# Kernel optimization log

Measured on AMD Instinct MI355X. Metric: run time of the kernel, lower is better.

The kernel has to match this reference:

```python
import jax, jax.numpy as jnp
import numpy as np

B, H, I, E, K = 512, 1024, 1024, 32, 4
EPS, ALPHA, LIMIT = 1e-5, 1.702, 7.0


def _swiglu(h):
    # interleaved split: even cols -> glu path, odd cols -> linear path
    x_glu = jnp.minimum(h[..., ::2], LIMIT)
    x_lin = jnp.clip(h[..., 1::2], -LIMIT, LIMIT)
    return x_glu * jax.nn.sigmoid(ALPHA * x_glu) * (x_lin + 1.0)


def setup_inputs() -> dict:
    key = jax.random.key(0)
    ks = jax.random.split(key, 7)
    n = lambda k, shape, s: jax.random.normal(k, shape, dtype=jnp.float32) * s
    return {
        "x": n(ks[0], (B, H), 1.0),
        "norm_scale": jnp.ones((H,), jnp.float32),
        "gate_w": n(ks[1], (E, H), 0.02),
        "gate_b": n(ks[2], (E,), 0.02),
        "mlp1_w": n(ks[3], (E, 2 * I, H), 0.02),
        "mlp1_b": n(ks[4], (E, 2 * I), 0.02),
        "mlp2_w": n(ks[5], (E, H, I), 0.02),
        "mlp2_b": n(ks[6], (E, H), 0.02),
    }


def reference(x, norm_scale, gate_w, gate_b, mlp1_w, mlp1_b, mlp2_w, mlp2_b):
    # RMSNorm in fp32
    t = x * jax.lax.rsqrt(jnp.mean(x * x, axis=-1, keepdims=True) + EPS) * norm_scale
    # gate + top-k routing; softmax over the k selected logits
    g = t @ gate_w.T + gate_b                      # [B, E]
    vals, idx = jax.lax.top_k(g, K)                # [B, K]
    w = jax.nn.softmax(vals, axis=-1)              # [B, K]
    # dense routing weights [B, E]: w_dense[b, e] = sum_k w[b,k] * (idx[b,k]==e)
    w_dense = jnp.zeros((t.shape[0], gate_w.shape[0]), t.dtype)
    w_dense = w_dense.at[jnp.arange(t.shape[0])[:, None], idx].add(w)
    # grouped-dense equivalent of the per-token gathered einsum:
    # original: einsum('beck,bk->bec', mlp1_w[idx], t); here we compute all
    # experts densely and combine with w_dense (zero for unselected experts),
    # which is the same math without materializing [B,K,2I,H] weights.
    h = jnp.einsum('bk,eck->bec', t, mlp1_w) + mlp1_b   # [B, E, 2I]
    a = _swiglu(h)                                       # [B, E, I]
    o = jnp.einsum('bei,ehi->beh', a, mlp2_w) + mlp2_b   # [B, E, H]
    y = jnp.einsum('beh,be->bh', o, w_dense)             # [B, H]
    return x + y
```

## Files before the change

kernel.cpp:

```cpp
#include <hip/hip_runtime.h>
#include <hip/hip_bf16.h>
#include <math.h>


#define NB   512
#define NH   1024
#define NI   1024
#define NE   32
#define NK   4
#define N2I  2048
#define CAP  512

static constexpr float EPS   = 1e-5f;
static constexpr float ALPHA = 1.702f;
static constexpr float LIMIT = 7.0f;

typedef short bf16x8 __attribute__((ext_vector_type(8)));
typedef float f32x4  __attribute__((ext_vector_type(4)));

__device__ __forceinline__ short hi16(float x) {
    return (short)(__float_as_uint(x) >> 16);
}
__device__ __forceinline__ short lo16(float x) {
    unsigned hb = __float_as_uint(x) & 0xFFFF0000u;
    float r = x - __uint_as_float(hb);
    return (short)(__float_as_uint(r) >> 16);
}
__device__ __forceinline__ void cvt8r(float4 v0, float4 v1,
                                      bf16x8& hh, bf16x8& ll) {
    float f[8] = {v0.x, v0.y, v0.z, v0.w, v1.x, v1.y, v1.z, v1.w};
#pragma unroll
    for (int i = 0; i < 8; i++) { hh[i] = hi16(f[i]); ll[i] = lo16(f[i]); }
}

__global__ __launch_bounds__(256) void k_rms_gate(
    const float* __restrict__ x, const float* __restrict__ scale,
    const float* __restrict__ gw, const float* __restrict__ gb,
    float* __restrict__ t, int* __restrict__ cnt,
    int* __restrict__ tok, int* __restrict__ tke, float* __restrict__ tkw) {
    __shared__ float sh_t[NH];
    __shared__ float sh_red[4];
    __shared__ float sh_g[NE];
    const int b = blockIdx.x, tid = threadIdx.x;
    const int lane = tid & 63, wid = tid >> 6;

    float4 xv = reinterpret_cast<const float4*>(x + (size_t)b * NH)[tid];
    float ss = xv.x * xv.x + xv.y * xv.y + xv.z * xv.z + xv.w * xv.w;
#pragma unroll
    for (int o = 32; o >= 1; o >>= 1) ss += __shfl_down(ss, o);
    if (lane == 0) sh_red[wid] = ss;
    __syncthreads();
    const float tot = sh_red[0] + sh_red[1] + sh_red[2] + sh_red[3];
    const float r = rsqrtf(tot * (1.0f / NH) + EPS);
    float4 sv = reinterpret_cast<const float4*>(scale)[tid];
    float4 tv;
    tv.x = xv.x * r * sv.x; tv.y = xv.y * r * sv.y;
    tv.z = xv.z * r * sv.z; tv.w = xv.w * r * sv.w;
    reinterpret_cast<float4*>(sh_t)[tid] = tv;
    reinterpret_cast<float4*>(t + (size_t)b * NH)[tid] = tv;
    __syncthreads();

#pragma unroll
    for (int q = 0; q < 8; q++) {
        const int e = wid * 8 + q;
        const float* __restrict__ w = gw + (size_t)e * NH;
        float p = 0.f;
#pragma unroll
        for (int i = 0; i < 16; i++) { int k = lane + 64 * i; p += sh_t[k] * w[k]; }
#pragma unroll
        for (int o = 32; o >= 1; o >>= 1) p += __shfl_down(p, o);
        if (lane == 0) sh_g[e] = p + gb[e];
    }
    __syncthreads();

    if (tid == 0) {
        float gv[NE];
#pragma unroll
        for (int e = 0; e < NE; e++) gv[e] = sh_g[e];
        float vals[NK]; int ids[NK];
#pragma unroll
        for (int k = 0; k < NK; k++) {
            int bi = 0; float bv = gv[0];
            for (int e = 1; e < NE; e++) if (gv[e] > bv) { bv = gv[e]; bi = e; }
            vals[k] = bv; ids[k] = bi; gv[bi] = -1e30f;
        }
        const float m = vals[0];
        float s = 0.f, wv[NK];
#pragma unroll
        for (int k = 0; k < NK; k++) { wv[k] = __expf(vals[k] - m); s += wv[k]; }
        const float inv = 1.f / s;
#pragma unroll
        for (int k = 0; k < NK; k++) {
            const int e = ids[k];
            const int pos = atomicAdd(&cnt[e], 1);
            tok[e * CAP + pos] = b;
            tke[b * NK + k] = (e << 16) | pos;
            tkw[b * NK + k] = wv[k] * inv;
        }
    }
}

__global__ void k_prefix(const int* __restrict__ cnt, int* __restrict__ base) {
    if (threadIdx.x == 0) {
        int r = 0;
        for (int e = 0; e < NE; e++) { base[e] = r; r += cnt[e]; }
    }
}

__global__ __launch_bounds__(256, 2) void k_mlp1(
    const float* __restrict__ t, const float* __restrict__ w1,
    const float* __restrict__ b1, const int* __restrict__ cnt,
    const int* __restrict__ base, const int* __restrict__ tok,
    float* __restrict__ a) {
    const int e  = blockIdx.z;
    const int ne = cnt[e];
    const int m0 = blockIdx.y * 128;
    if (m0 >= ne) return;
    const int c0 = blockIdx.x * 128;
    const float* __restrict__ W = w1 + (size_t)e * N2I * NH + (size_t)c0 * NH;

    __shared__ short Ah[128][72], Al[128][72];
    __shared__ short Bh[128][72], Bl[128][72];
    __shared__ int   toks[128];

    const int tid = threadIdx.x;
    if (tid < 128) toks[tid] = (m0 + tid < ne) ? tok[e * CAP + m0 + tid] : -1;
    __syncthreads();

    const int lane = tid & 63;
    const int wv   = tid >> 6;
    const int wr = wv >> 1, wc = wv & 1;
    const int frow = lane & 15;
    const int fk   = (lane >> 4) * 8;
    const int sr = tid >> 3;
    const int sg = (tid & 7) * 8;

    f32x4 acc[4][4] = {};
    float4 ra[4][2], rb[4][2];
    int tkr[4];

#pragma unroll
    for (int p = 0; p < 4; p++) {
        const int r = sr + 32 * p;
        const int tk = toks[r]; tkr[p] = tk;
        const float* src = t + (size_t)(tk < 0 ? 0 : tk) * NH + sg;
        ra[p][0] = *(const float4*)src;
        ra[p][1] = *(const float4*)(src + 4);
        const float* wsrc = W + (size_t)r * NH + sg;
        rb[p][0] = *(const float4*)wsrc;
        rb[p][1] = *(const float4*)(wsrc + 4);
    }

    for (int k0 = 0; k0 < NH; k0 += 64) {
#pragma unroll
        for (int p = 0; p < 4; p++) {
            const int r = sr + 32 * p;
            bf16x8 hh, ll;
            cvt8r(ra[p][0], ra[p][1], hh, ll);
            if (tkr[p] < 0) {
#pragma unroll
                for (int i = 0; i < 8; i++) { hh[i] = 0; ll[i] = 0; }
            }
            *(bf16x8*)&Ah[r][sg] = hh;
            *(bf16x8*)&Al[r][sg] = ll;
            cvt8r(rb[p][0], rb[p][1], hh, ll);
            *(bf16x8*)&Bh[r][sg] = hh;
            *(bf16x8*)&Bl[r][sg] = ll;
        }
        if (k0 + 64 < NH) {
            const int kn = k0 + 64;
#pragma unroll
            for (int p = 0; p < 4; p++) {
                const int r = sr + 32 * p;
                const int tk = tkr[p];
                const float* src = t + (size_t)(tk < 0 ? 0 : tk) * NH + kn + sg;
                ra[p][0] = *(const float4*)src;
                ra[p][1] = *(const float4*)(src + 4);
                const float* wsrc = W + (size_t)r * NH + kn + sg;
                rb[p][0] = *(const float4*)wsrc;
                rb[p][1] = *(const float4*)(wsrc + 4);
            }
        }
        __syncthreads();
#pragma unroll
        for (int kk = 0; kk < 64; kk += 32) {
            bf16x8 ah[4], al[4], bh[4], bl[4];
#pragma unroll
            for (int m = 0; m < 4; m++) {
                const int r = wr * 64 + m * 16 + frow;
                ah[m] = *(const bf16x8*)&Ah[r][kk + fk];
                al[m] = *(const bf16x8*)&Al[r][kk + fk];
            }
#pragma unroll
            for (int n = 0; n < 4; n++) {
                const int c = wc * 64 + n * 16 + frow;
                bh[n] = *(const bf16x8*)&Bh[c][kk + fk];
                bl[n] = *(const bf16x8*)&Bl[c][kk + fk];
            }
#pragma unroll
            for (int m = 0; m < 4; m++)
#pragma unroll
                for (int n = 0; n < 4; n++) {
                    acc[m][n] = __builtin_amdgcn_mfma_f32_16x16x32_bf16(ah[m], bh[n], acc[m][n], 0, 0, 0);
                    acc[m][n] = __builtin_amdgcn_mfma_f32_16x16x32_bf16(ah[m], bl[n], acc[m][n], 0, 0, 0);
                    acc[m][n] = __builtin_amdgcn_mfma_f32_16x16x32_bf16(al[m], bh[n], acc[m][n], 0, 0, 0);
                }
        }
        __syncthreads();
    }

    const int slot0 = base[e];
#pragma unroll
    for (int m = 0; m < 4; m++)
#pragma unroll
        for (int n = 0; n < 4; n++) {
            const int gcol = c0 + wc * 64 + n * 16 + frow;
            const float bias = b1[e * N2I + gcol];
            f32x4 v = acc[m][n];
#pragma unroll
            for (int j = 0; j < 4; j++) {
                const float h  = v[j] + bias;
                const float hp = __shfl_xor(h, 1);
                const int row = m0 + wr * 64 + m * 16 + (lane >> 4) * 4 + j;
                if (!(lane & 1) && row < ne) {
                    const float xg = fminf(h, LIMIT);
                    const float xl = fminf(fmaxf(hp, -LIMIT), LIMIT);
                    const float sg2 = 1.f / (1.f + __expf(-ALPHA * xg));
                    a[(size_t)(slot0 + row) * NI + (gcol >> 1)] = xg * sg2 * (xl + 1.f);
                }
            }
        }
}

__global__ __launch_bounds__(256, 2) void k_mlp2(
    const float* __restrict__ a, const float* __restrict__ w2,
    const float* __restrict__ b2, const int* __restrict__ cnt,
    const int* __restrict__ base, float* __restrict__ o) {
    const int e  = blockIdx.z;
    const int ne = cnt[e];
    const int m0 = blockIdx.y * 128;
    if (m0 >= ne) return;
    const int c0 = blockIdx.x * 128;
    const int slot0 = base[e];
    const float* __restrict__ W = w2 + (size_t)e * NH * NI + (size_t)c0 * NI;

    __shared__ short Ah[128][72], Al[128][72];
    __shared__ short Bh[128][72], Bl[128][72];

    const int tid = threadIdx.x;
    const int lane = tid & 63;
    const int wv   = tid >> 6;
    const int wr = wv >> 1, wc = wv & 1;
    const int frow = lane & 15;
    const int fk   = (lane >> 4) * 8;
    const int sr = tid >> 3;
    const int sg = (tid & 7) * 8;

    f32x4 acc[4][4] = {};
    float4 ra[4][2], rb[4][2];
    int mv[4];

#pragma unroll
    for (int p = 0; p < 4; p++) {
        const int r = sr + 32 * p;
        const int m = m0 + r;
        mv[p] = (m < ne);
        const float* src = a + (size_t)(mv[p] ? (slot0 + m) : 0) * NI + sg;
        ra[p][0] = *(const float4*)src;
        ra[p][1] = *(const float4*)(src + 4);
        const float* wsrc = W + (size_t)r * NI + sg;
        rb[p][0] = *(const float4*)wsrc;
        rb[p][1] = *(const float4*)(wsrc + 4);
    }

    for (int k0 = 0; k0 < NI; k0 += 64) {
#pragma unroll
        for (int p = 0; p < 4; p++) {
            const int r = sr + 32 * p;
            bf16x8 hh, ll;
            cvt8r(ra[p][0], ra[p][1], hh, ll);
            if (!mv[p]) {
#pragma unroll
                for (int i = 0; i < 8; i++) { hh[i] = 0; ll[i] = 0; }
            }
            *(bf16x8*)&Ah[r][sg] = hh;
            *(bf16x8*)&Al[r][sg] = ll;
            cvt8r(rb[p][0], rb[p][1], hh, ll);
            *(bf16x8*)&Bh[r][sg] = hh;
            *(bf16x8*)&Bl[r][sg] = ll;
        }
        if (k0 + 64 < NI) {
            const int kn = k0 + 64;
#pragma unroll
            for (int p = 0; p < 4; p++) {
                const int r = sr + 32 * p;
                const int m = m0 + r;
                const float* src = a + (size_t)(mv[p] ? (slot0 + m) : 0) * NI + kn + sg;
                ra[p][0] = *(const float4*)src;
                ra[p][1] = *(const float4*)(src + 4);
                const float* wsrc = W + (size_t)r * NI + kn + sg;
                rb[p][0] = *(const float4*)wsrc;
                rb[p][1] = *(const float4*)(wsrc + 4);
            }
        }
        __syncthreads();
#pragma unroll
        for (int kk = 0; kk < 64; kk += 32) {
            bf16x8 ah[4], al[4], bh[4], bl[4];
#pragma unroll
            for (int m = 0; m < 4; m++) {
                const int r = wr * 64 + m * 16 + frow;
                ah[m] = *(const bf16x8*)&Ah[r][kk + fk];
                al[m] = *(const bf16x8*)&Al[r][kk + fk];
            }
#pragma unroll
            for (int n = 0; n < 4; n++) {
                const int c = wc * 64 + n * 16 + frow;
                bh[n] = *(const bf16x8*)&Bh[c][kk + fk];
                bl[n] = *(const bf16x8*)&Bl[c][kk + fk];
            }
#pragma unroll
            for (int m = 0; m < 4; m++)
#pragma unroll
                for (int n = 0; n < 4; n++) {
                    acc[m][n] = __builtin_amdgcn_mfma_f32_16x16x32_bf16(ah[m], bh[n], acc[m][n], 0, 0, 0);
                    acc[m][n] = __builtin_amdgcn_mfma_f32_16x16x32_bf16(ah[m], bl[n], acc[m][n], 0, 0, 0);
                    acc[m][n] = __builtin_amdgcn_mfma_f32_16x16x32_bf16(al[m], bh[n], acc[m][n], 0, 0, 0);
                }
        }
        __syncthreads();
    }

#pragma unroll
    for (int m = 0; m < 4; m++)
#pragma unroll
        for (int n = 0; n < 4; n++) {
            const int gcol = c0 + wc * 64 + n * 16 + frow;
            const float bias = b2[e * NH + gcol];
            f32x4 v = acc[m][n];
#pragma unroll
            for (int j = 0; j < 4; j++) {
                const int row = m0 + wr * 64 + m * 16 + (lane >> 4) * 4 + j;
                if (row < ne)
                    o[(size_t)(slot0 + row) * NH + gcol] = v[j] + bias;
            }
        }
}

__global__ __launch_bounds__(256) void k_combine(
    const float* __restrict__ x, const float* __restrict__ o,
    const int* __restrict__ base, const int* __restrict__ tke,
    const float* __restrict__ tkw, float* __restrict__ out) {
    const int b = blockIdx.x, tid = threadIdx.x;
    int slots[NK]; float wk[NK];
#pragma unroll
    for (int k = 0; k < NK; k++) {
        const int v = tke[b * NK + k];
        slots[k] = base[v >> 16] + (v & 0xFFFF);
        wk[k] = tkw[b * NK + k];
    }
    float4 r = reinterpret_cast<const float4*>(x + (size_t)b * NH)[tid];
#pragma unroll
    for (int k = 0; k < NK; k++) {
        float4 ov = reinterpret_cast<const float4*>(o + (size_t)slots[k] * NH)[tid];
        r.x += wk[k] * ov.x; r.y += wk[k] * ov.y;
        r.z += wk[k] * ov.z; r.w += wk[k] * ov.w;
    }
    reinterpret_cast<float4*>(out + (size_t)b * NH)[tid] = r;
}

extern "C" void kernel_launch(void* const* d_in, const int* in_sizes, int n_in,
                              void* d_out, int out_size, void* d_ws, size_t ws_size,
                              hipStream_t stream) {
    const float* x     = (const float*)d_in[0];
    const float* scale = (const float*)d_in[1];
    const float* gw    = (const float*)d_in[2];
    const float* gb    = (const float*)d_in[3];
    const float* w1    = (const float*)d_in[4];
    const float* b1    = (const float*)d_in[5];
    const float* w2    = (const float*)d_in[6];
    const float* b2    = (const float*)d_in[7];
    float* out = (float*)d_out;

    float* t   = (float*)d_ws;
    float* a   = t + (size_t)NB * NH;
    float* o   = a + (size_t)NB * NK * NI;
    int*   tok = (int*)(o + (size_t)NB * NK * NH);
    int*   tke = tok + NE * CAP;
    float* tkw = (float*)(tke + NB * NK);
    int*   cnt = (int*)(tkw + NB * NK);
    int*   bse = cnt + NE;

    hipMemsetAsync(cnt, 0, NE * sizeof(int), stream);
    k_rms_gate<<<NB, 256, 0, stream>>>(x, scale, gw, gb, t, cnt, tok, tke, tkw);
    k_prefix<<<1, 64, 0, stream>>>(cnt, bse);
    k_mlp1<<<dim3(N2I / 128, NB / 128, NE), 256, 0, stream>>>(t, w1, b1, cnt, bse, tok, a);
    k_mlp2<<<dim3(NH / 128, NB / 128, NE), 256, 0, stream>>>(a, w2, b2, cnt, bse, o);
    k_combine<<<NB, 256, 0, stream>>>(x, o, bse, tke, tkw, out);
}
```

Measured before the change: 611.1 us.

## Use 512-thread blocks with 8 warps and K-step 32 in MLP GEMMs

Both expert GEMM kernels move from 4 warps with 64x64 per-warp tiles to 8 warps with 32x64 per-warp tiles. The shared-memory K chunk shrinks from 64 to 32 (padded row width 40), and each thread now stages a single row segment instead of four. The aim is to cut per-thread register pressure and raise the number of resident waves, so memory latency is hidden better. In exchange there are twice as many barrier-separated iterations, each with less MFMA work, and A-fragment reuse across the N dimension per warp is lower.

Result: faster. 598.6 us (-2.0%).

```diff
diff --git a/kernel.cpp b/kernel.cpp
--- a/kernel.cpp
+++ b/kernel.cpp
@@ -10,6 +10,7 @@
 #define NK   4
 #define N2I  2048
 #define CAP  512
+#define PADK 40
 
 static constexpr float EPS   = 1e-5f;
 static constexpr float ALPHA = 1.702f;
@@ -107,7 +108,7 @@
     }
 }
 
-__global__ __launch_bounds__(256, 2) void k_mlp1(
+__global__ __launch_bounds__(512, 2) void k_mlp1(
     const float* __restrict__ t, const float* __restrict__ w1,
     const float* __restrict__ b1, const int* __restrict__ cnt,
     const int* __restrict__ base, const int* __restrict__ tok,
@@ -119,8 +120,8 @@
     const int c0 = blockIdx.x * 128;
     const float* __restrict__ W = w1 + (size_t)e * N2I * NH + (size_t)c0 * NH;
 
-    __shared__ short Ah[128][72], Al[128][72];
-    __shared__ short Bh[128][72], Bl[128][72];
+    __shared__ short Ah[128][PADK], Al[128][PADK];
+    __shared__ short Bh[128][PADK], Bl[128][PADK];
     __shared__ int   toks[128];
 
     const int tid = threadIdx.x;
@@ -128,90 +129,68 @@
     __syncthreads();
 
     const int lane = tid & 63;
-    const int wv   = tid >> 6;
-    const int wr = wv >> 1, wc = wv & 1;
+    const int wid  = tid >> 6;
+    const int wr = wid >> 1, wc = wid & 1;
     const int frow = lane & 15;
     const int fk   = (lane >> 4) * 8;
-    const int sr = tid >> 3;
-    const int sg = (tid & 7) * 8;
-
-    f32x4 acc[4][4] = {};
-    float4 ra[4][2], rb[4][2];
-    int tkr[4];
-
-#pragma unroll
-    for (int p = 0; p < 4; p++) {
-        const int r = sr + 32 * p;
-        const int tk = toks[r]; tkr[p] = tk;
-        const float* src = t + (size_t)(tk < 0 ? 0 : tk) * NH + sg;
-        ra[p][0] = *(const float4*)src;
-        ra[p][1] = *(const float4*)(src + 4);
-        const float* wsrc = W + (size_t)r * NH + sg;
-        rb[p][0] = *(const float4*)wsrc;
-        rb[p][1] = *(const float4*)(wsrc + 4);
-    }
-
-    for (int k0 = 0; k0 < NH; k0 += 64) {
-#pragma unroll
-        for (int p = 0; p < 4; p++) {
-            const int r = sr + 32 * p;
-            bf16x8 hh, ll;
-            cvt8r(ra[p][0], ra[p][1], hh, ll);
-            if (tkr[p] < 0) {
-#pragma unroll
-                for (int i = 0; i < 8; i++) { hh[i] = 0; ll[i] = 0; }
+    const int srow = tid >> 2;
+    const int sc8  = (tid & 3) * 8;
+
+    f32x4 acc[2][4] = {};
+
+    const int tka = toks[srow];
+    const float* __restrict__ asrc = t + (size_t)(tka < 0 ? 0 : tka) * NH + sc8;
+    const float* __restrict__ bsrc = W + (size_t)srow * NH + sc8;
+
+    float4 ra0 = *(const float4*)(asrc);
+    float4 ra1 = *(const float4*)(asrc + 4);
+    float4 rb0 = *(const float4*)(bsrc);
+    float4 rb1 = *(const float4*)(bsrc + 4);
+
+    for (int k0 = 0; k0 < NH; k0 += 32) {
+        bf16x8 hh, ll;
+        cvt8r(ra0, ra1, hh, ll);
+        if (tka < 0) { hh = (bf16x8)(short)0; ll = (bf16x8)(short)0; }
+        *(bf16x8*)&Ah[srow][sc8] = hh;
+        *(bf16x8*)&Al[srow][sc8] = ll;
+        cvt8r(rb0, rb1, hh, ll);
+        *(bf16x8*)&Bh[srow][sc8] = hh;
+        *(bf16x8*)&Bl[srow][sc8] = ll;
+        if (k0 + 32 < NH) {
+            ra0 = *(const float4*)(asrc + k0 + 32);
+            ra1 = *(const float4*)(asrc + k0 + 36);
+            rb0 = *(const float4*)(bsrc + k0 + 32);
+            rb1 = *(const float4*)(bsrc + k0 + 36);
+        }
+        __syncthreads();
+
+        bf16x8 ah[2], al[2], bh[4], bl[4];
+#pragma unroll
+        for (int m = 0; m < 2; m++) {
+            const int r = wr * 32 + m * 16 + frow;
+            ah[m] = *(const bf16x8*)&Ah[r][fk];
+            al[m] = *(const bf16x8*)&Al[r][fk];
+        }
+#pragma unroll
+        for (int n = 0; n < 4; n++) {
+            const int c = wc * 64 + n * 16 + frow;
+            bh[n] = *(const bf16x8*)&Bh[c][fk];
+            bl[n] = *(const bf16x8*)&Bl[c][fk];
+        }
+#pragma unroll
+        for (int m = 0; m < 2; m++)
+#pragma unroll
+            for (int n = 0; n < 4; n++) {
+                acc[m][n] = __builtin_amdgcn_mfma_f32_16x16x32_bf16(ah[m], bh[n], acc[m][n], 0, 0, 0);
+                acc[m][n] = __builtin_amdgcn_mfma_f32_16x16x32_bf16(ah[m], bl[n], acc[m][n], 0, 0, 0);
+                acc[m][n] = __builtin_amdgcn_mfma_f32_16x16x32_bf16(al[m], bh[n], acc[m][n], 0, 0, 0);
             }
-            *(bf16x8*)&Ah[r][sg] = hh;
-            *(bf16x8*)&Al[r][sg] = ll;
-            cvt8r(rb[p][0], rb[p][1], hh, ll);
-            *(bf16x8*)&Bh[r][sg] = hh;
-            *(bf16x8*)&Bl[r][sg] = ll;
-        }
-        if (k0 + 64 < NH) {
-            const int kn = k0 + 64;
-#pragma unroll
-            for (int p = 0; p < 4; p++) {
-                const int r = sr + 32 * p;
-                const int tk = tkr[p];
-                const float* src = t + (size_t)(tk < 0 ? 0 : tk) * NH + kn + sg;
-                ra[p][0] = *(const float4*)src;
-                ra[p][1] = *(const float4*)(src + 4);
-                const float* wsrc = W + (size_t)r * NH + kn + sg;
-                rb[p][0] = *(const float4*)wsrc;
-                rb[p][1] = *(const float4*)(wsrc + 4);
-            }
-        }
         __syncthreads();
-#pragma unroll
-        for (int kk = 0; kk < 64; kk += 32) {
-            bf16x8 ah[4], al[4], bh[4], bl[4];
-#pragma unroll
-            for (int m = 0; m < 4; m++) {
-                const int r = wr * 64 + m * 16 + frow;
-                ah[m] = *(const bf16x8*)&Ah[r][kk + fk];
-                al[m] = *(const bf16x8*)&Al[r][kk + fk];
-            }
-#pragma unroll
-            for (int n = 0; n < 4; n++) {
-                const int c = wc * 64 + n * 16 + frow;
-                bh[n] = *(const bf16x8*)&Bh[c][kk + fk];
-                bl[n] = *(const bf16x8*)&Bl[c][kk + fk];
-            }
-#pragma unroll
-            for (int m = 0; m < 4; m++)
-#pragma unroll
-                for (int n = 0; n < 4; n++) {
-                    acc[m][n] = __builtin_amdgcn_mfma_f32_16x16x32_bf16(ah[m], bh[n], acc[m][n], 0, 0, 0);
-                    acc[m][n] = __builtin_amdgcn_mfma_f32_16x16x32_bf16(ah[m], bl[n], acc[m][n], 0, 0, 0);
-                    acc[m][n] = __builtin_amdgcn_mfma_f32_16x16x32_bf16(al[m], bh[n], acc[m][n], 0, 0, 0);
-                }
-        }
-        __syncthreads();
     }
 
     const int slot0 = base[e];
 #pragma unroll
-    for (int m = 0; m < 4; m++)
+    for (int m = 0; m < 2; m++)
 #pragma unroll
         for (int n = 0; n < 4; n++) {
             const int gcol = c0 + wc * 64 + n * 16 + frow;
@@ -221,7 +200,7 @@
             for (int j = 0; j < 4; j++) {
                 const float h  = v[j] + bias;
                 const float hp = __shfl_xor(h, 1);
-                const int row = m0 + wr * 64 + m * 16 + (lane >> 4) * 4 + j;
+                const int row = m0 + wr * 32 + m * 16 + (lane >> 4) * 4 + j;
                 if (!(lane & 1) && row < ne) {
                     const float xg = fminf(h, LIMIT);
                     const float xl = fminf(fmaxf(hp, -LIMIT), LIMIT);
@@ -232,7 +211,7 @@
         }
 }
 
-__global__ __launch_bounds__(256, 2) void k_mlp2(
+__global__ __launch_bounds__(512, 2) void k_mlp2(
     const float* __restrict__ a, const float* __restrict__ w2,
     const float* __restrict__ b2, const int* __restrict__ cnt,
     const int* __restrict__ base, float* __restrict__ o) {
@@ -244,95 +223,73 @@
     const int slot0 = base[e];
     const float* __restrict__ W = w2 + (size_t)e * NH * NI + (size_t)c0 * NI;
 
-    __shared__ short Ah[128][72], Al[128][72];
-    __shared__ short Bh[128][72], Bl[128][72];
+    __shared__ short Ah[128][PADK], Al[128][PADK];
+    __shared__ short Bh[128][PADK], Bl[128][PADK];
 
     const int tid = threadIdx.x;
     const int lane = tid & 63;
-    const int wv   = tid >> 6;
-    const int wr = wv >> 1, wc = wv & 1;
+    const int wid  = tid >> 6;
+    const int wr = wid >> 1, wc = wid & 1;
     const int frow = lane & 15;
     const int fk   = (lane >> 4) * 8;
-    const int sr = tid >> 3;
-    const int sg = (tid & 7) * 8;
-
-    f32x4 acc[4][4] = {};
-    float4 ra[4][2], rb[4][2];
-    int mv[4];
-
-#pragma unroll
-    for (int p = 0; p < 4; p++) {
-        const int r = sr + 32 * p;
-        const int m = m0 + r;
-        mv[p] = (m < ne);
-        const float* src = a + (size_t)(mv[p] ? (slot0 + m) : 0) * NI + sg;
-        ra[p][0] = *(const float4*)src;
-        ra[p][1] = *(const float4*)(src + 4);
-        const float* wsrc = W + (size_t)r * NI + sg;
-        rb[p][0] = *(const float4*)wsrc;
-        rb[p][1] = *(const float4*)(wsrc + 4);
-    }
-
-    for (int k0 = 0; k0 < NI; k0 += 64) {
-#pragma unroll
-        for (int p = 0; p < 4; p++) {
-            const int r = sr + 32 * p;
-            bf16x8 hh, ll;
-            cvt8r(ra[p][0], ra[p][1], hh, ll);
-            if (!mv[p]) {
-#pragma unroll
-                for (int i = 0; i < 8; i++) { hh[i] = 0; ll[i] = 0; }
+    const int srow = tid >> 2;
+    const int sc8  = (tid & 3) * 8;
+
+    f32x4 acc[2][4] = {};
+
+    const int mval = (m0 + srow < ne);
+    const float* __restrict__ asrc =
+        a + (size_t)(mval ? (slot0 + m0 + srow) : 0) * NI + sc8;
+    const float* __restrict__ bsrc = W + (size_t)srow * NI + sc8;
+
+    float4 ra0 = *(const float4*)(asrc);
+    float4 ra1 = *(const float4*)(asrc + 4);
+    float4 rb0 = *(const float4*)(bsrc);
+    float4 rb1 = *(const float4*)(bsrc + 4);
+
+    for (int k0 = 0; k0 < NI; k0 += 32) {
+        bf16x8 hh, ll;
+        cvt8r(ra0, ra1, hh, ll);
+        if (!mval) { hh = (bf16x8)(short)0; ll = (bf16x8)(short)0; }
+        *(bf16x8*)&Ah[srow][sc8] = hh;
+        *(bf16x8*)&Al[srow][sc8] = ll;
+        cvt8r(rb0, rb1, hh, ll);
+        *(bf16x8*)&Bh[srow][sc8] = hh;
+        *(bf16x8*)&Bl[srow][sc8] = ll;
+        if (k0 + 32 < NI) {
+            ra0 = *(const float4*)(asrc + k0 + 32);
+            ra1 = *(const float4*)(asrc + k0 + 36);
+            rb0 = *(const float4*)(bsrc + k0 + 32);
+            rb1 = *(const float4*)(bsrc + k0 + 36);
+        }
+        __syncthreads();
+
+        bf16x8 ah[2], al[2], bh[4], bl[4];
+#pragma unroll
+        for (int m = 0; m < 2; m++) {
+            const int r = wr * 32 + m * 16 + frow;
+            ah[m] = *(const bf16x8*)&Ah[r][fk];
+            al[m] = *(const bf16x8*)&Al[r][fk];
+        }
+#pragma unroll
+        for (int n = 0; n < 4; n++) {
+            const int c = wc * 64 + n * 16 + frow;
+            bh[n] = *(const bf16x8*)&Bh[c][fk];
+            bl[n] = *(const bf16x8*)&Bl[c][fk];
+        }
+#pragma unroll
+        for (int m = 0; m < 2; m++)
+#pragma unroll
+            for (int n = 0; n < 4; n++) {
+                acc[m][n] = __builtin_amdgcn_mfma_f32_16x16x32_bf16(ah[m], bh[n], acc[m][n], 0, 0, 0);
+                acc[m][n] = __builtin_amdgcn_mfma_f32_16x16x32_bf16(ah[m], bl[n], acc[m][n], 0, 0, 0);
+                acc[m][n] = __builtin_amdgcn_mfma_f32_16x16x32_bf16(al[m], bh[n], acc[m][n], 0, 0, 0);
             }
-            *(bf16x8*)&Ah[r][sg] = hh;
-            *(bf16x8*)&Al[r][sg] = ll;
-            cvt8r(rb[p][0], rb[p][1], hh, ll);
-            *(bf16x8*)&Bh[r][sg] = hh;
-            *(bf16x8*)&Bl[r][sg] = ll;
-        }
-        if (k0 + 64 < NI) {
-            const int kn = k0 + 64;
-#pragma unroll
-            for (int p = 0; p < 4; p++) {
-                const int r = sr + 32 * p;
-                const int m = m0 + r;
-                const float* src = a + (size_t)(mv[p] ? (slot0 + m) : 0) * NI + kn + sg;
-                ra[p][0] = *(const float4*)src;
-                ra[p][1] = *(const float4*)(src + 4);
-                const float* wsrc = W + (size_t)r * NI + kn + sg;
-                rb[p][0] = *(const float4*)wsrc;
-                rb[p][1] = *(const float4*)(wsrc + 4);
-            }
-        }
         __syncthreads();
-#pragma unroll
-        for (int kk = 0; kk < 64; kk += 32) {
-            bf16x8 ah[4], al[4], bh[4], bl[4];
-#pragma unroll
-            for (int m = 0; m < 4; m++) {
-                const int r = wr * 64 + m * 16 + frow;
-                ah[m] = *(const bf16x8*)&Ah[r][kk + fk];
-                al[m] = *(const bf16x8*)&Al[r][kk + fk];
-            }
-#pragma unroll
-            for (int n = 0; n < 4; n++) {
-                const int c = wc * 64 + n * 16 + frow;
-                bh[n] = *(const bf16x8*)&Bh[c][kk + fk];
-                bl[n] = *(const bf16x8*)&Bl[c][kk + fk];
-            }
-#pragma unroll
-            for (int m = 0; m < 4; m++)
-#pragma unroll
-                for (int n = 0; n < 4; n++) {
-                    acc[m][n] = __builtin_amdgcn_mfma_f32_16x16x32_bf16(ah[m], bh[n], acc[m][n], 0, 0, 0);
-                    acc[m][n] = __builtin_amdgcn_mfma_f32_16x16x32_bf16(ah[m], bl[n], acc[m][n], 0, 0, 0);
-                    acc[m][n] = __builtin_amdgcn_mfma_f32_16x16x32_bf16(al[m], bh[n], acc[m][n], 0, 0, 0);
-                }
-        }
-        __syncthreads();
-    }
-
-#pragma unroll
-    for (int m = 0; m < 4; m++)
+    }
+
+#pragma unroll
+    for (int m = 0; m < 2; m++)
 #pragma unroll
         for (int n = 0; n < 4; n++) {
             const int gcol = c0 + wc * 64 + n * 16 + frow;
@@ -340,7 +297,7 @@
             f32x4 v = acc[m][n];
 #pragma unroll
             for (int j = 0; j < 4; j++) {
-                const int row = m0 + wr * 64 + m * 16 + (lane >> 4) * 4 + j;
+                const int row = m0 + wr * 32 + m * 16 + (lane >> 4) * 4 + j;
                 if (row < ne)
                     o[(size_t)(slot0 + row) * NH + gcol] = v[j] + bias;
             }
@@ -394,7 +351,7 @@
     hipMemsetAsync(cnt, 0, NE * sizeof(int), stream);
     k_rms_gate<<<NB, 256, 0, stream>>>(x, scale, gw, gb, t, cnt, tok, tke, tkw);
     k_prefix<<<1, 64, 0, stream>>>(cnt, bse);
-    k_mlp1<<<dim3(N2I / 128, NB / 128, NE), 256, 0, stream>>>(t, w1, b1, cnt, bse, tok, a);
-    k_mlp2<<<dim3(NH / 128, NB / 128, NE), 256, 0, stream>>>(a, w2, b2, cnt, bse, o);
+    k_mlp1<<<dim3(N2I / 128, NB / 128, NE), 512, 0, stream>>>(t, w1, b1, cnt, bse, tok, a);
+    k_mlp2<<<dim3(NH / 128, NB / 128, NE), 512, 0, stream>>>(a, w2, b2, cnt, bse, o);
     k_combine<<<NB, 256, 0, stream>>>(x, o, bse, tke, tkw, out);
 }
```
